# Optimization experiments

Hardware: AMD Instinct MI355X
Metric: run time of the kernel (lower is better)

Reference implementation:

```python
import jax, jax.numpy as jnp
import numpy as np
from jax import lax

B, C, H, W = 4096, 10, 30, 30
NCOL = C - 1                      # non-background colors 1..9
_pi, _pj = np.triu_indices(NCOL, 1)  # lexicographic (i<j) pair order, matches the python double loop
PI = jnp.asarray(_pi); PJ = jnp.asarray(_pj)
NPAIR = int(_pi.shape[0])         # 36
W_TRANSFORM, W_EXACT, W_AFFINE, W_ROT, W_REFL, W_GEO, W_EDGE, W_CBAL = 0.2, 7.0, 0.4, 0.3, 0.3, 0.5, 0.3, 0.2
GAMMA = 1.4


def setup_inputs() -> dict:
    key = jax.random.key(0)
    ks = jax.random.split(key, 6)
    pred = jax.random.normal(ks[0], (B, C, H, W), jnp.float32)
    tidx = jax.random.randint(ks[1], (B, H, W), 0, C)
    target = jnp.transpose(jax.nn.one_hot(tidx, C, dtype=jnp.float32), (0, 3, 1, 2))
    iidx = jax.random.randint(ks[2], (B, H, W), 0, C)
    input_grid = jnp.transpose(jax.nn.one_hot(iidx, C, dtype=jnp.float32), (0, 3, 1, 2))
    theta = 0.1 * jax.random.normal(ks[3], (B, 2, 3), jnp.float32)
    rot = jax.random.normal(ks[4], (B, 8), jnp.float32)
    refl = jax.random.normal(ks[5], (B, 4), jnp.float32)
    return {"pred_output": pred, "target_output": target, "input_grid": input_grid,
            "theta": theta, "rotation_logits": rot, "reflection_logits": refl}


def _detect_edges(idx):
    # idx: [B,H,W] int; pixel is an edge if it differs from any h/w neighbor
    dh = idx[:, 1:, :] != idx[:, :-1, :]
    dw = idx[:, :, 1:] != idx[:, :, :-1]
    e = jnp.pad(dh, ((0, 0), (1, 0), (0, 0))) | jnp.pad(dh, ((0, 0), (0, 1), (0, 0)))
    e = e | jnp.pad(dw, ((0, 0), (0, 0), (1, 0))) | jnp.pad(dw, ((0, 0), (0, 0), (0, 1)))
    return e


def _entropy_mean(logits):
    lp = jax.nn.log_softmax(logits, axis=1)
    return (-(jnp.exp(lp) * lp).sum(axis=1)).mean()


def _sobel(idx_f):
    sx = jnp.array([[-1., 0., 1.], [-2., 0., 2.], [-1., 0., 1.]], jnp.float32).reshape(1, 1, 3, 3)
    sy = jnp.array([[-1., -2., -1.], [0., 0., 0.], [1., 2., 1.]], jnp.float32).reshape(1, 1, 3, 3)
    x = idx_f[:, None]  # [B,1,H,W]
    dn = ('NCHW', 'OIHW', 'NCHW')
    ex = lax.conv_general_dilated(x, sx, (1, 1), ((1, 1), (1, 1)), dimension_numbers=dn)
    ey = lax.conv_general_dilated(x, sy, (1, 1), ((1, 1), (1, 1)), dimension_numbers=dn)
    return jnp.sqrt(ex * ex + ey * ey)


def _centers(grid):
    # grid: [H,W] int -> per-color (1..9) center of mass and presence
    cols = jnp.arange(1, C)
    mask = (grid[None] == cols[:, None, None]).astype(jnp.float32)  # [9,H,W]
    cnt = mask.sum((1, 2))
    ys = jnp.arange(H, dtype=jnp.float32)[:, None]
    xs = jnp.arange(W, dtype=jnp.float32)[None, :]
    cy = (mask * ys).sum((1, 2)) / jnp.maximum(cnt, 1.0)
    cx = (mask * xs).sum((1, 2)) / jnp.maximum(cnt, 1.0)
    return cy, cx, cnt > 0


def _compact_dists(cy, cx, present):
    # distances for all 36 color pairs, compacted so valid pairs occupy
    # the leading slots in the same lexicographic order as the torch loops
    d = jnp.sqrt((cy[PI] - cy[PJ]) ** 2 + (cx[PI] - cx[PJ]) ** 2)
    v = present[PI] & present[PJ]
    rank = jnp.cumsum(v.astype(jnp.int32)) - 1
    slot = jnp.where(v, rank, NPAIR)          # dump invalid pairs in scratch slot
    compact = jnp.zeros(NPAIR + 1, jnp.float32).at[slot].set(d)
    return compact[:NPAIR], v.sum()


def _geo_sample(pidx, tidx):
    cyp, cxp, prp = _centers(pidx)
    cyt, cxt, prt = _centers(tidx)
    dp, n_p = _compact_dists(cyp, cxp, prp)
    dt, n_t = _compact_dists(cyt, cxt, prt)
    m = jnp.minimum(n_p, n_t)                 # min_len truncation
    use = jnp.arange(NPAIR) < m
    sq = jnp.where(use, (dp - dt) ** 2, 0.0)
    return jnp.where(m > 0, sq.sum() / jnp.maximum(m, 1).astype(jnp.float32), 0.0)


def _components(pred, target, inp, theta, rot, refl):
    tidx = jnp.argmax(target, axis=1)
    pidx = jnp.argmax(pred, axis=1)
    iidx = jnp.argmax(inp, axis=1)
    # spatial focal CE with edge-weighted pixels
    lp = jax.nn.log_softmax(pred, axis=1)
    ce = -jnp.take_along_axis(lp, tidx[:, None], axis=1)[:, 0]  # [B,H,W]
    pt = jnp.exp(-ce)
    sw = jnp.where(_detect_edges(tidx), 1.5, 1.0)
    spatial_focal = ((1.0 - pt) ** GAMMA * ce * sw).mean()
    # exact match bonus / copy penalty
    exact = jnp.all(pidx == tidx, axis=(1, 2)).astype(jnp.float32)
    exact_count = exact.sum()
    exact_bonus = -exact.mean() * W_EXACT
    copy = jnp.all(pidx == iidx, axis=(1, 2)).astype(jnp.float32)
    transform = copy.mean() * W_TRANSFORM
    # affine regularization on theta
    scale_reg = jnp.sqrt((theta[:, :2, :2] ** 2).sum((1, 2)))
    trans_reg = jnp.sqrt((theta[:, :, 2] ** 2).sum(1))
    affine = (scale_reg.mean() + 0.1 * trans_reg.mean()) * W_AFFINE
    rotation = _entropy_mean(rot) * W_ROT
    reflection = _entropy_mean(refl) * W_REFL
    # geometric color-center consistency (vmapped over batch)
    geo = jax.vmap(_geo_sample)(pidx, tidx).sum() / B * W_GEO
    # sobel edge MSE on argmax indices
    pe = _sobel(pidx.astype(jnp.float32))
    te = _sobel(tidx.astype(jnp.float32))
    edge = jnp.mean((pe - te) ** 2) * W_EDGE
    # color balance
    pc = jax.nn.softmax(pred, axis=1).sum((2, 3))
    tc = target.sum((2, 3))
    pc = pc / (pc.sum(1, keepdims=True) + 1e-8)
    tc = tc / (tc.sum(1, keepdims=True) + 1e-8)
    cbal = jnp.mean((pc - tc) ** 2) * W_CBAL
    total = (spatial_focal + transform + affine + rotation + reflection
             + geo + edge + cbal + exact_bonus)
    return (total, spatial_focal, transform, exact_bonus, exact_count,
            affine, rotation, reflection, geo, edge, cbal)


def reference(pred_output, target_output, input_grid, theta, rotation_logits, reflection_logits):
    return _components(pred_output, target_output, input_grid, theta,
                       rotation_logits, reflection_logits)
```

## Files before the change

kernel.cpp:

```cpp
#include <hip/hip_runtime.h>
#include <stdint.h>

#define B_   4096
#define C_   10
#define H_   30
#define W_   30
#define HW_  900
#define NCOL_ 9
#define NPART 9

typedef float f32x4 __attribute__((ext_vector_type(4)));


__device__ __forceinline__ float entropyN(const float* __restrict__ x, int n) {
    float m = x[0];
    for (int i = 1; i < n; ++i) m = fmaxf(m, x[i]);
    float se = 0.f;
    for (int i = 0; i < n; ++i) se += __expf(x[i] - m);
    float lse = m + __logf(se);
    float ent = 0.f;
    for (int i = 0; i < n; ++i) { float lp = x[i] - lse; ent -= __expf(lp) * lp; }
    return ent;
}

template <int CTRL>
__device__ __forceinline__ float dpp_add_stage(float x) {
    int y = __builtin_amdgcn_update_dpp(0, __builtin_bit_cast(int, x),
                                        CTRL, 0xf, 0xf, true);
    return x + __builtin_bit_cast(float, y);
}
__device__ __forceinline__ float wave_sum64(float x) {
    x = dpp_add_stage<0x111>(x);
    x = dpp_add_stage<0x112>(x);
    x = dpp_add_stage<0x114>(x);
    x = dpp_add_stage<0x118>(x);
    x = dpp_add_stage<0x142>(x);
    x = dpp_add_stage<0x143>(x);
    return __builtin_bit_cast(float,
        __builtin_amdgcn_readlane(__builtin_bit_cast(int, x), 63));
}


__global__ __launch_bounds__(64) void zero_out_k(float* out, int n) {
    int i = threadIdx.x;
    if (i < n) out[i] = 0.f;
}

__global__ __launch_bounds__(256, 3) void loss_main(
    const float* __restrict__ pred, const float* __restrict__ target,
    const float* __restrict__ inp,  const float* __restrict__ theta,
    const float* __restrict__ rotl, const float* __restrict__ refl,
    float* __restrict__ partials ,
    float* __restrict__ out)
{
    __shared__ uint8_t s_t[33 * 32];
    __shared__ uint8_t s_p[33 * 32];
    __shared__ __align__(16) float s_fb[30 * 36];
    __shared__ unsigned long long s_ctr[2][NCOL_];
    __shared__ float s_wred[4][16];
    __shared__ float s_dp[36], s_dt[36];
    __shared__ float s_cy[2][NCOL_], s_cx[2][NCOL_];
    __shared__ int   s_pr[2][NCOL_];
    __shared__ int   s_tcnt[NCOL_];
    __shared__ float s_small[4];

    const int t    = threadIdx.x;
    const int wid  = t >> 6;
    const int lane = t & 63;
    const int b    = blockIdx.x;
    const size_t base = (size_t)b * (C_ * HW_);

    float pc[C_];
#pragma unroll
    for (int c = 0; c < C_; ++c) pc[c] = 0.f;
    float focal_base = 0.f, focal_edge = 0.f, edg = 0.f;
    bool ok_e = true, ok_c = true;

    if (t < 225) {
        const int p0 = 4 * t;
        const float* pp = pred   + base + p0;
        const float* tp = target + base + p0;
        const float* gp = inp    + base + p0;

        f32x4 pfv[C_], tfv[C_], gfv[C_];
#pragma unroll
        for (int c = 0; c < C_; ++c)
            asm volatile("global_load_dwordx4 %0, %1, off"
                         : "=v"(pfv[c]) : "v"(pp + c * HW_));
#pragma unroll
        for (int c = 0; c < C_; ++c)
            asm volatile("global_load_dwordx4 %0, %1, off"
                         : "=v"(tfv[c]) : "v"(tp + c * HW_));
#pragma unroll
        for (int c = 0; c < C_; ++c)
            asm volatile("global_load_dwordx4 %0, %1, off"
                         : "=v"(gfv[c]) : "v"(gp + c * HW_));
        asm volatile("s_waitcnt vmcnt(0)" ::: "memory");
        __builtin_amdgcn_sched_barrier(0);

        float vt[4]  = {0.f, 0.f, 0.f, 0.f};
        float tif[4] = {0.f, 0.f, 0.f, 0.f};
        float iif[4] = {0.f, 0.f, 0.f, 0.f};
#pragma unroll
        for (int c = 0; c < C_; ++c) {
            const f32x4 tf = tfv[c];
            const f32x4 pf = pfv[c];
            const f32x4 gf = gfv[c];
            const float fc = (float)c;
            vt[0] = fmaf(tf.x, pf.x, vt[0]); vt[1] = fmaf(tf.y, pf.y, vt[1]);
            vt[2] = fmaf(tf.z, pf.z, vt[2]); vt[3] = fmaf(tf.w, pf.w, vt[3]);
            tif[0] = fmaf(tf.x, fc, tif[0]); tif[1] = fmaf(tf.y, fc, tif[1]);
            tif[2] = fmaf(tf.z, fc, tif[2]); tif[3] = fmaf(tf.w, fc, tif[3]);
            iif[0] = fmaf(gf.x, fc, iif[0]); iif[1] = fmaf(gf.y, fc, iif[1]);
            iif[2] = fmaf(gf.z, fc, iif[2]); iif[3] = fmaf(gf.w, fc, iif[3]);
        }

        int h = p0 / 30;
        int w = p0 - 30 * h;
#pragma unroll
        for (int j = 0; j < 4; ++j) {
            const int ti = (int)tif[j];
            const int ii = (int)iif[j];
            float pm = pfv[0][j]; int pi = 0;
            float se = 0.f;
            float ex[C_];
#pragma unroll
            for (int c = 0; c < C_; ++c) {
                const float raw = pfv[c][j];
                if (c > 0 && raw > pm) { pm = raw; pi = c; }
                float e = __expf(raw);
                ex[c] = e;
                se += e;
            }
            const float inv = __builtin_amdgcn_rcpf(se);
#pragma unroll
            for (int c = 0; c < C_; ++c) pc[c] = fmaf(ex[c], inv, pc[c]);
            const float ce = __logf(se) - vt[j];
            const float pt = __expf(-ce);
            const float omt = fmaxf(1.f - pt, 0.f);
            const float fb = __powf(omt, 1.4f) * ce;
            focal_base += fb;

            s_t[(h + 1) * 32 + (w + 1)] = (uint8_t)ti;
            s_p[(h + 1) * 32 + (w + 1)] = (uint8_t)pi;
            s_fb[36 * h + w] = fb;
            if (pi != ti) ok_e = false;
            if (pi != ii) ok_c = false;
            if (++w == 30) { w = 0; ++h; }
        }
    } else if (t < 252) {
        const int z = t - 225;
        for (int k = z; k < 32; k += 27) {
            const int g = k >> 4, r = (k >> 3) & 1, dw = k & 7;
            uint32_t* pb = (uint32_t*)((g ? s_p : s_t) + (r ? 31 * 32 : 0));
            pb[dw] = 0u;
        }
        for (int k = z; k < 120; k += 27) {
            const int g = (k >= 60);
            const int kk = k - 60 * g;
            const int r = 1 + (kk >> 1);
            const int cp = (kk & 1) ? 31 : 0;
            (g ? s_p : s_t)[r * 32 + cp] = 0;
        }
        for (int k = z; k < 2 * NCOL_; k += 27) ((unsigned long long*)s_ctr)[k] = 0ull;
    } else if (t == 252) {
        s_small[0] = entropyN(rotl + (size_t)b * 8, 8);
    } else if (t == 253) {
        s_small[1] = entropyN(refl + (size_t)b * 4, 4);
    } else if (t == 254) {
        const float* th = theta + (size_t)b * 6;
        float sreg = sqrtf(th[0]*th[0] + th[1]*th[1] + th[3]*th[3] + th[4]*th[4]);
        float treg = sqrtf(th[2]*th[2] + th[5]*th[5]);
        s_small[2] = sreg + 0.1f * treg;
    }
    __syncthreads();

    if (t < 240) {
        const int h = t >> 3, wq = t & 7;
        const int w0 = 4 * wq;
        const int npx = (w0 < 28) ? 4 : 2;

        const uint32_t* tr0 = (const uint32_t*)(s_t + 32 * h);
        const uint32_t* tr1 = (const uint32_t*)(s_t + 32 * (h + 1));
        const uint32_t* tr2 = (const uint32_t*)(s_t + 32 * (h + 2));
        const uint32_t* pr0 = (const uint32_t*)(s_p + 32 * h);
        const uint32_t* pr1 = (const uint32_t*)(s_p + 32 * (h + 1));
        const uint32_t* pr2 = (const uint32_t*)(s_p + 32 * (h + 2));

        uint32_t td[3][2] = {{tr0[wq], tr0[wq + 1]}, {tr1[wq], tr1[wq + 1]}, {tr2[wq], tr2[wq + 1]}};
        uint32_t pd[3][2] = {{pr0[wq], pr0[wq + 1]}, {pr1[wq], pr1[wq + 1]}, {pr2[wq], pr2[wq + 1]}};
        const float4 fbf = *reinterpret_cast<const float4*>(s_fb + 36 * h + w0);
        const float fbarr[4] = {fbf.x, fbf.y, fbf.z, fbf.w};

        int tb2[3][6], pb2[3][6];
#pragma unroll
        for (int r = 0; r < 3; ++r) {
            const uint32_t d0t = td[r][0], d1t = td[r][1];
            tb2[r][0] = d0t & 255; tb2[r][1] = (d0t >> 8) & 255; tb2[r][2] = (d0t >> 16) & 255;
            tb2[r][3] = d0t >> 24; tb2[r][4] = d1t & 255; tb2[r][5] = (d1t >> 8) & 255;
            const uint32_t d0p = pd[r][0], d1p = pd[r][1];
            pb2[r][0] = d0p & 255; pb2[r][1] = (d0p >> 8) & 255; pb2[r][2] = (d0p >> 16) & 255;
            pb2[r][3] = d0p >> 24; pb2[r][4] = d1p & 255; pb2[r][5] = (d1p >> 8) & 255;
        }
        int s1t[6], s2t[6], s1p[6], s2p[6];
#pragma unroll
        for (int j = 0; j < 6; ++j) {
            s1t[j] = tb2[0][j] + 2 * tb2[1][j] + tb2[2][j];
            s2t[j] = tb2[2][j] - tb2[0][j];
            s1p[j] = pb2[0][j] + 2 * pb2[1][j] + pb2[2][j];
            s2p[j] = pb2[2][j] - pb2[0][j];
        }
#pragma unroll
        for (int k = 0; k < 4; ++k) {
            if (k < npx) {
                const int w = w0 + k;
                const int tv = tb2[1][k + 1], pv2 = pb2[1][k + 1];
                const bool eg = (h > 0  && tb2[0][k + 1] != tv) ||
                                (h < 29 && tb2[2][k + 1] != tv) ||
                                (w > 0  && tb2[1][k]     != tv) ||
                                (w < 29 && tb2[1][k + 2] != tv);
                if (eg) focal_edge += fbarr[k];

                const int ext = s1t[k + 2] - s1t[k];
                const int eyt = s2t[k] + 2 * s2t[k + 1] + s2t[k + 2];
                const int exq = s1p[k + 2] - s1p[k];
                const int eyq = s2p[k] + 2 * s2p[k + 1] + s2p[k + 2];
                const float mt = sqrtf((float)(ext * ext + eyt * eyt));
                const float mp = sqrtf((float)(exq * exq + eyq * eyq));
                const float dd = mp - mt;
                edg += dd * dd;

                const unsigned long long add =
                    (1ull << 42) | ((unsigned long long)(unsigned)h << 21) | (unsigned)w;
                if (tv  > 0) atomicAdd(&s_ctr[1][tv  - 1], add);
                if (pv2 > 0) atomicAdd(&s_ctr[0][pv2 - 1], add);
            }
        }
    }

    float vals[12];
    vals[0] = focal_base + 0.5f * focal_edge;
    vals[1] = edg;
#pragma unroll
    for (int c = 0; c < C_; ++c) vals[2 + c] = pc[c];
#pragma unroll
    for (int k = 0; k < 12; ++k) vals[k] = wave_sum64(vals[k]);
    const int all_e = __all(ok_e);
    const int all_c = __all(ok_c);
    if (lane == 0) {
#pragma unroll
        for (int k = 0; k < 12; ++k) s_wred[wid][k] = vals[k];
        s_wred[wid][12] = (float)all_e;
        s_wred[wid][13] = (float)all_c;
    }
    __syncthreads();

    if (t < 18) {
        const int g = (t >= 9);
        const int k = t - 9 * g;
        const unsigned long long q = s_ctr[g][k];
        const int sx = (int)(q & 0x1FFFFF), sy = (int)((q >> 21) & 0x1FFFFF), cn = (int)(q >> 42);
        const float dn = fmaxf((float)cn, 1.f);
        s_cy[g][k] = (float)sy / dn;
        s_cx[g][k] = (float)sx / dn;
        s_pr[g][k] = (cn > 0);
        if (g) s_tcnt[k] = cn;
    }
    __syncthreads();

    if (t < 64) {
        const int l = t;
        const int i = (l >= 8) + (l >= 15) + (l >= 21) + (l >= 26) +
                      (l >= 30) + (l >= 33) + (l >= 35);
        const int j = l - (i * (17 - i)) / 2 + i + 1;
        bool vp = false, vtp = false;
        float dp = 0.f, dt = 0.f;
        if (l < 36) {
            vp  = s_pr[0][i] && s_pr[0][j];
            vtp = s_pr[1][i] && s_pr[1][j];
            float dyp = s_cy[0][i] - s_cy[0][j], dxp = s_cx[0][i] - s_cx[0][j];
            dp = sqrtf(dyp * dyp + dxp * dxp);
            float dyt = s_cy[1][i] - s_cy[1][j], dxt = s_cx[1][i] - s_cx[1][j];
            dt = sqrtf(dyt * dyt + dxt * dxt);
        }
        const unsigned long long mp_mask = __ballot(vp);
        const unsigned long long mt_mask = __ballot(vtp);
        const unsigned long long below = (1ull << l) - 1ull;
        if (vp)  s_dp[__popcll(mp_mask & below)] = dp;
        if (vtp) s_dt[__popcll(mt_mask & below)] = dt;
        const int np = (int)__popcll(mp_mask);
        const int nt = (int)__popcll(mt_mask);
        const int mm = np < nt ? np : nt;
        asm volatile("s_waitcnt lgkmcnt(0)" ::: "memory");
        __builtin_amdgcn_wave_barrier();
        float term = 0.f;
        if (l < mm) { float d = s_dp[l] - s_dt[l]; term = d * d; }
#pragma unroll
        for (int off = 32; off > 0; off >>= 1) term += __shfl_down(term, off);

        if (t == 0) {
            const float geo_b = (mm > 0) ? term / (float)mm : 0.f;

            float r[14];
#pragma unroll
            for (int k = 0; k < 14; ++k) r[k] = s_wred[0][k];
            for (int w2 = 1; w2 < 4; ++w2) {
#pragma unroll
                for (int k = 0; k < 12; ++k) r[k] += s_wred[w2][k];
                r[12] = fminf(r[12], s_wred[w2][12]);
                r[13] = fminf(r[13], s_wred[w2][13]);
            }

            float pcs = 0.f;
#pragma unroll
            for (int c = 0; c < C_; ++c) pcs += r[2 + c];
            const float ipcs = 1.f / (pcs + 1e-8f);
            int tsum = 0;
#pragma unroll
            for (int k = 0; k < NCOL_; ++k) tsum += s_tcnt[k];
            float cb = 0.f;
            const float itd = 1.f / (900.f + 1e-8f);
            {
                float d = r[2] * ipcs - (float)(HW_ - tsum) * itd;
                cb += d * d;
            }
#pragma unroll
            for (int c = 1; c < C_; ++c) {
                float d = r[2 + c] * ipcs - (float)s_tcnt[c - 1] * itd;
                cb += d * d;
            }

            float res[NPART];
            res[0] = r[0];
            res[1] = r[12];
            res[2] = r[13];
            res[3] = s_small[2];
            res[4] = s_small[0];
            res[5] = s_small[1];
            res[6] = geo_b;
            res[7] = r[1];
            res[8] = cb;

            if (partials) {
                float* pw = partials + (size_t)b * NPART;
#pragma unroll
                for (int k = 0; k < NPART; ++k) pw[k] = res[k];
            } else {
                atomicAdd(&out[1],  res[0]);
                atomicAdd(&out[2],  res[2]);
                atomicAdd(&out[4],  res[1]);
                atomicAdd(&out[5],  res[3]);
                atomicAdd(&out[6],  res[4]);
                atomicAdd(&out[7],  res[5]);
                atomicAdd(&out[8],  res[6]);
                atomicAdd(&out[9],  res[7]);
                atomicAdd(&out[10], res[8]);
            }
        }
    }
}

__device__ __forceinline__ void write_final(float* out,
    double focal_s, double exact_s, double copy_s, double aff_s,
    double rot_s, double refl_s, double geo_s, double edge_s, double cbal_s)
{
    const double invB = 1.0 / (double)B_;
    float focal      = (float)(focal_s / ((double)B_ * (double)HW_));
    float transform  = (float)(copy_s * invB * 0.2);
    float exact_cnt  = (float)exact_s;
    float exact_bns  = (float)(-(exact_s * invB) * 7.0);
    float affine     = (float)(aff_s * invB * 0.4);
    float rotation   = (float)(rot_s * invB * 0.3);
    float reflection = (float)(refl_s * invB * 0.3);
    float geo        = (float)(geo_s * invB * 0.5);
    float edge       = (float)(edge_s / ((double)B_ * (double)HW_) * 0.3);
    float cbal       = (float)(cbal_s / ((double)B_ * (double)C_) * 0.2);
    out[0] = focal + transform + affine + rotation + reflection + geo + edge + cbal + exact_bns;
    out[1] = focal; out[2] = transform; out[3] = exact_bns; out[4] = exact_cnt;
    out[5] = affine; out[6] = rotation; out[7] = reflection; out[8] = geo;
    out[9] = edge; out[10] = cbal;
}

__global__ __launch_bounds__(256) void reduce_partials(
    const float* __restrict__ partials, float* __restrict__ out)
{
    __shared__ double sh[256][NPART];
    const int t = threadIdx.x;
    double acc[NPART];
#pragma unroll
    for (int k = 0; k < NPART; ++k) acc[k] = 0.0;
    for (int b = t; b < B_; b += 256) {
        const float* pp = partials + (size_t)b * NPART;
#pragma unroll
        for (int k = 0; k < NPART; ++k) acc[k] += (double)pp[k];
    }
#pragma unroll
    for (int k = 0; k < NPART; ++k) sh[t][k] = acc[k];
    __syncthreads();
    for (int s = 128; s > 0; s >>= 1) {
        if (t < s) {
#pragma unroll
            for (int k = 0; k < NPART; ++k) sh[t][k] += sh[t + s][k];
        }
        __syncthreads();
    }
    if (t == 0) {
        write_final(out, sh[0][0], sh[0][1], sh[0][2], sh[0][3],
                    sh[0][4], sh[0][5], sh[0][6], sh[0][7], sh[0][8]);
    }
}

__global__ void finalize_atomic(float* out) {
    if (threadIdx.x == 0) {
        write_final(out, (double)out[1], (double)out[4], (double)out[2], (double)out[5],
                    (double)out[6], (double)out[7], (double)out[8], (double)out[9],
                    (double)out[10]);
    }
}


extern "C" void kernel_launch(void* const* d_in, const int* in_sizes, int n_in,
                              void* d_out, int out_size, void* d_ws, size_t ws_size,
                              hipStream_t stream) {
    const float* pred   = (const float*)d_in[0];
    const float* target = (const float*)d_in[1];
    const float* inp    = (const float*)d_in[2];
    const float* theta  = (const float*)d_in[3];
    const float* rotl   = (const float*)d_in[4];
    const float* refl   = (const float*)d_in[5];
    float* out = (float*)d_out;

    const size_t need = (size_t)B_ * NPART * sizeof(float);
    if (d_ws != nullptr && ws_size >= need) {
        loss_main<<<B_, 256, 0, stream>>>(pred, target, inp, theta, rotl, refl,
                                          (float*)d_ws, out);
        reduce_partials<<<1, 256, 0, stream>>>((const float*)d_ws, out);
    } else {
        zero_out_k<<<1, 64, 0, stream>>>(out, out_size);
        loss_main<<<B_, 256, 0, stream>>>(pred, target, inp, theta, rotl, refl,
                                          nullptr, out);
        finalize_atomic<<<1, 1, 0, stream>>>(out);
    }
}
```

Baseline: 89.65 us.

## Process four batch elements per block with prefetch of next element's loads

Each block now handles four batch samples in a loop. As soon as the per-pixel phase of one sample finishes, it issues the global loads for the next sample, so those loads overlap the stencil, atomic and reduction phases. Loads are split so pred and target are waited on first and the input grid later. The launch bound drops to two blocks per CU and the grid shrinks by four. This trades fewer resident blocks and more register pressure for overlap on what is likely a bandwidth-bound kernel.

```diff
diff --git a/kernel.cpp b/kernel.cpp
--- a/kernel.cpp
+++ b/kernel.cpp
@@ -1,13 +1,14 @@
 #include <hip/hip_runtime.h>
 #include <stdint.h>
 
-#define B_   4096
-#define C_   10
-#define H_   30
-#define W_   30
-#define HW_  900
+#define B_    4096
+#define C_    10
+#define H_    30
+#define W_    30
+#define HW_   900
 #define NCOL_ 9
 #define NPART 9
+#define ELEMS 4
 
 typedef float f32x4 __attribute__((ext_vector_type(4)));
 
@@ -46,7 +47,7 @@
     if (i < n) out[i] = 0.f;
 }
 
-__global__ __launch_bounds__(256, 3) void loss_main(
+__global__ __launch_bounds__(256, 2) void loss_main(
     const float* __restrict__ pred, const float* __restrict__ target,
     const float* __restrict__ inp,  const float* __restrict__ theta,
     const float* __restrict__ rotl, const float* __restrict__ refl,
@@ -62,27 +63,20 @@
     __shared__ float s_cy[2][NCOL_], s_cx[2][NCOL_];
     __shared__ int   s_pr[2][NCOL_];
     __shared__ int   s_tcnt[NCOL_];
-    __shared__ float s_small[4];
+    __shared__ float s_small[ELEMS][4];
 
     const int t    = threadIdx.x;
     const int wid  = t >> 6;
     const int lane = t & 63;
-    const int b    = blockIdx.x;
-    const size_t base = (size_t)b * (C_ * HW_);
-
-    float pc[C_];
-#pragma unroll
-    for (int c = 0; c < C_; ++c) pc[c] = 0.f;
-    float focal_base = 0.f, focal_edge = 0.f, edg = 0.f;
-    bool ok_e = true, ok_c = true;
-
-    if (t < 225) {
-        const int p0 = 4 * t;
-        const float* pp = pred   + base + p0;
-        const float* tp = target + base + p0;
-        const float* gp = inp    + base + p0;
-
-        f32x4 pfv[C_], tfv[C_], gfv[C_];
+    const int b0   = blockIdx.x * ELEMS;
+    const int p0   = 4 * t;
+
+    f32x4 pfv[C_], tfv[C_], gfv[C_];
+
+    auto issue = [&](size_t bs) {
+        const float* pp = pred   + bs + p0;
+        const float* tp = target + bs + p0;
+        const float* gp = inp    + bs + p0;
 #pragma unroll
         for (int c = 0; c < C_; ++c)
             asm volatile("global_load_dwordx4 %0, %1, off"
@@ -95,59 +89,10 @@
         for (int c = 0; c < C_; ++c)
             asm volatile("global_load_dwordx4 %0, %1, off"
                          : "=v"(gfv[c]) : "v"(gp + c * HW_));
-        asm volatile("s_waitcnt vmcnt(0)" ::: "memory");
-        __builtin_amdgcn_sched_barrier(0);
-
-        float vt[4]  = {0.f, 0.f, 0.f, 0.f};
-        float tif[4] = {0.f, 0.f, 0.f, 0.f};
-        float iif[4] = {0.f, 0.f, 0.f, 0.f};
-#pragma unroll
-        for (int c = 0; c < C_; ++c) {
-            const f32x4 tf = tfv[c];
-            const f32x4 pf = pfv[c];
-            const f32x4 gf = gfv[c];
-            const float fc = (float)c;
-            vt[0] = fmaf(tf.x, pf.x, vt[0]); vt[1] = fmaf(tf.y, pf.y, vt[1]);
-            vt[2] = fmaf(tf.z, pf.z, vt[2]); vt[3] = fmaf(tf.w, pf.w, vt[3]);
-            tif[0] = fmaf(tf.x, fc, tif[0]); tif[1] = fmaf(tf.y, fc, tif[1]);
-            tif[2] = fmaf(tf.z, fc, tif[2]); tif[3] = fmaf(tf.w, fc, tif[3]);
-            iif[0] = fmaf(gf.x, fc, iif[0]); iif[1] = fmaf(gf.y, fc, iif[1]);
-            iif[2] = fmaf(gf.z, fc, iif[2]); iif[3] = fmaf(gf.w, fc, iif[3]);
-        }
-
-        int h = p0 / 30;
-        int w = p0 - 30 * h;
-#pragma unroll
-        for (int j = 0; j < 4; ++j) {
-            const int ti = (int)tif[j];
-            const int ii = (int)iif[j];
-            float pm = pfv[0][j]; int pi = 0;
-            float se = 0.f;
-            float ex[C_];
-#pragma unroll
-            for (int c = 0; c < C_; ++c) {
-                const float raw = pfv[c][j];
-                if (c > 0 && raw > pm) { pm = raw; pi = c; }
-                float e = __expf(raw);
-                ex[c] = e;
-                se += e;
-            }
-            const float inv = __builtin_amdgcn_rcpf(se);
-#pragma unroll
-            for (int c = 0; c < C_; ++c) pc[c] = fmaf(ex[c], inv, pc[c]);
-            const float ce = __logf(se) - vt[j];
-            const float pt = __expf(-ce);
-            const float omt = fmaxf(1.f - pt, 0.f);
-            const float fb = __powf(omt, 1.4f) * ce;
-            focal_base += fb;
-
-            s_t[(h + 1) * 32 + (w + 1)] = (uint8_t)ti;
-            s_p[(h + 1) * 32 + (w + 1)] = (uint8_t)pi;
-            s_fb[36 * h + w] = fb;
-            if (pi != ti) ok_e = false;
-            if (pi != ii) ok_c = false;
-            if (++w == 30) { w = 0; ++h; }
-        }
+    };
+
+    if (t < 225) {
+        issue((size_t)b0 * (C_ * HW_));
     } else if (t < 252) {
         const int z = t - 225;
         for (int k = z; k < 32; k += 27) {
@@ -162,199 +107,287 @@
             const int cp = (kk & 1) ? 31 : 0;
             (g ? s_p : s_t)[r * 32 + cp] = 0;
         }
-        for (int k = z; k < 2 * NCOL_; k += 27) ((unsigned long long*)s_ctr)[k] = 0ull;
     } else if (t == 252) {
-        s_small[0] = entropyN(rotl + (size_t)b * 8, 8);
+#pragma unroll
+        for (int e = 0; e < ELEMS; ++e)
+            s_small[e][0] = entropyN(rotl + (size_t)(b0 + e) * 8, 8);
     } else if (t == 253) {
-        s_small[1] = entropyN(refl + (size_t)b * 4, 4);
+#pragma unroll
+        for (int e = 0; e < ELEMS; ++e)
+            s_small[e][1] = entropyN(refl + (size_t)(b0 + e) * 4, 4);
     } else if (t == 254) {
-        const float* th = theta + (size_t)b * 6;
-        float sreg = sqrtf(th[0]*th[0] + th[1]*th[1] + th[3]*th[3] + th[4]*th[4]);
-        float treg = sqrtf(th[2]*th[2] + th[5]*th[5]);
-        s_small[2] = sreg + 0.1f * treg;
-    }
-    __syncthreads();
-
-    if (t < 240) {
-        const int h = t >> 3, wq = t & 7;
-        const int w0 = 4 * wq;
-        const int npx = (w0 < 28) ? 4 : 2;
-
-        const uint32_t* tr0 = (const uint32_t*)(s_t + 32 * h);
-        const uint32_t* tr1 = (const uint32_t*)(s_t + 32 * (h + 1));
-        const uint32_t* tr2 = (const uint32_t*)(s_t + 32 * (h + 2));
-        const uint32_t* pr0 = (const uint32_t*)(s_p + 32 * h);
-        const uint32_t* pr1 = (const uint32_t*)(s_p + 32 * (h + 1));
-        const uint32_t* pr2 = (const uint32_t*)(s_p + 32 * (h + 2));
-
-        uint32_t td[3][2] = {{tr0[wq], tr0[wq + 1]}, {tr1[wq], tr1[wq + 1]}, {tr2[wq], tr2[wq + 1]}};
-        uint32_t pd[3][2] = {{pr0[wq], pr0[wq + 1]}, {pr1[wq], pr1[wq + 1]}, {pr2[wq], pr2[wq + 1]}};
-        const float4 fbf = *reinterpret_cast<const float4*>(s_fb + 36 * h + w0);
-        const float fbarr[4] = {fbf.x, fbf.y, fbf.z, fbf.w};
-
-        int tb2[3][6], pb2[3][6];
-#pragma unroll
-        for (int r = 0; r < 3; ++r) {
-            const uint32_t d0t = td[r][0], d1t = td[r][1];
-            tb2[r][0] = d0t & 255; tb2[r][1] = (d0t >> 8) & 255; tb2[r][2] = (d0t >> 16) & 255;
-            tb2[r][3] = d0t >> 24; tb2[r][4] = d1t & 255; tb2[r][5] = (d1t >> 8) & 255;
-            const uint32_t d0p = pd[r][0], d1p = pd[r][1];
-            pb2[r][0] = d0p & 255; pb2[r][1] = (d0p >> 8) & 255; pb2[r][2] = (d0p >> 16) & 255;
-            pb2[r][3] = d0p >> 24; pb2[r][4] = d1p & 255; pb2[r][5] = (d1p >> 8) & 255;
-        }
-        int s1t[6], s2t[6], s1p[6], s2p[6];
-#pragma unroll
-        for (int j = 0; j < 6; ++j) {
-            s1t[j] = tb2[0][j] + 2 * tb2[1][j] + tb2[2][j];
-            s2t[j] = tb2[2][j] - tb2[0][j];
-            s1p[j] = pb2[0][j] + 2 * pb2[1][j] + pb2[2][j];
-            s2p[j] = pb2[2][j] - pb2[0][j];
-        }
-#pragma unroll
-        for (int k = 0; k < 4; ++k) {
-            if (k < npx) {
-                const int w = w0 + k;
-                const int tv = tb2[1][k + 1], pv2 = pb2[1][k + 1];
-                const bool eg = (h > 0  && tb2[0][k + 1] != tv) ||
-                                (h < 29 && tb2[2][k + 1] != tv) ||
-                                (w > 0  && tb2[1][k]     != tv) ||
-                                (w < 29 && tb2[1][k + 2] != tv);
-                if (eg) focal_edge += fbarr[k];
-
-                const int ext = s1t[k + 2] - s1t[k];
-                const int eyt = s2t[k] + 2 * s2t[k + 1] + s2t[k + 2];
-                const int exq = s1p[k + 2] - s1p[k];
-                const int eyq = s2p[k] + 2 * s2p[k + 1] + s2p[k + 2];
-                const float mt = sqrtf((float)(ext * ext + eyt * eyt));
-                const float mp = sqrtf((float)(exq * exq + eyq * eyq));
-                const float dd = mp - mt;
-                edg += dd * dd;
-
-                const unsigned long long add =
-                    (1ull << 42) | ((unsigned long long)(unsigned)h << 21) | (unsigned)w;
-                if (tv  > 0) atomicAdd(&s_ctr[1][tv  - 1], add);
-                if (pv2 > 0) atomicAdd(&s_ctr[0][pv2 - 1], add);
-            }
-        }
-    }
-
-    float vals[12];
-    vals[0] = focal_base + 0.5f * focal_edge;
-    vals[1] = edg;
-#pragma unroll
-    for (int c = 0; c < C_; ++c) vals[2 + c] = pc[c];
-#pragma unroll
-    for (int k = 0; k < 12; ++k) vals[k] = wave_sum64(vals[k]);
-    const int all_e = __all(ok_e);
-    const int all_c = __all(ok_c);
-    if (lane == 0) {
-#pragma unroll
-        for (int k = 0; k < 12; ++k) s_wred[wid][k] = vals[k];
-        s_wred[wid][12] = (float)all_e;
-        s_wred[wid][13] = (float)all_c;
-    }
-    __syncthreads();
-
-    if (t < 18) {
-        const int g = (t >= 9);
-        const int k = t - 9 * g;
-        const unsigned long long q = s_ctr[g][k];
-        const int sx = (int)(q & 0x1FFFFF), sy = (int)((q >> 21) & 0x1FFFFF), cn = (int)(q >> 42);
-        const float dn = fmaxf((float)cn, 1.f);
-        s_cy[g][k] = (float)sy / dn;
-        s_cx[g][k] = (float)sx / dn;
-        s_pr[g][k] = (cn > 0);
-        if (g) s_tcnt[k] = cn;
-    }
-    __syncthreads();
-
-    if (t < 64) {
-        const int l = t;
-        const int i = (l >= 8) + (l >= 15) + (l >= 21) + (l >= 26) +
-                      (l >= 30) + (l >= 33) + (l >= 35);
-        const int j = l - (i * (17 - i)) / 2 + i + 1;
-        bool vp = false, vtp = false;
-        float dp = 0.f, dt = 0.f;
-        if (l < 36) {
-            vp  = s_pr[0][i] && s_pr[0][j];
-            vtp = s_pr[1][i] && s_pr[1][j];
-            float dyp = s_cy[0][i] - s_cy[0][j], dxp = s_cx[0][i] - s_cx[0][j];
-            dp = sqrtf(dyp * dyp + dxp * dxp);
-            float dyt = s_cy[1][i] - s_cy[1][j], dxt = s_cx[1][i] - s_cx[1][j];
-            dt = sqrtf(dyt * dyt + dxt * dxt);
-        }
-        const unsigned long long mp_mask = __ballot(vp);
-        const unsigned long long mt_mask = __ballot(vtp);
-        const unsigned long long below = (1ull << l) - 1ull;
-        if (vp)  s_dp[__popcll(mp_mask & below)] = dp;
-        if (vtp) s_dt[__popcll(mt_mask & below)] = dt;
-        const int np = (int)__popcll(mp_mask);
-        const int nt = (int)__popcll(mt_mask);
-        const int mm = np < nt ? np : nt;
-        asm volatile("s_waitcnt lgkmcnt(0)" ::: "memory");
-        __builtin_amdgcn_wave_barrier();
-        float term = 0.f;
-        if (l < mm) { float d = s_dp[l] - s_dt[l]; term = d * d; }
-#pragma unroll
-        for (int off = 32; off > 0; off >>= 1) term += __shfl_down(term, off);
-
-        if (t == 0) {
-            const float geo_b = (mm > 0) ? term / (float)mm : 0.f;
-
-            float r[14];
-#pragma unroll
-            for (int k = 0; k < 14; ++k) r[k] = s_wred[0][k];
-            for (int w2 = 1; w2 < 4; ++w2) {
-#pragma unroll
-                for (int k = 0; k < 12; ++k) r[k] += s_wred[w2][k];
-                r[12] = fminf(r[12], s_wred[w2][12]);
-                r[13] = fminf(r[13], s_wred[w2][13]);
-            }
-
-            float pcs = 0.f;
-#pragma unroll
-            for (int c = 0; c < C_; ++c) pcs += r[2 + c];
-            const float ipcs = 1.f / (pcs + 1e-8f);
-            int tsum = 0;
-#pragma unroll
-            for (int k = 0; k < NCOL_; ++k) tsum += s_tcnt[k];
-            float cb = 0.f;
-            const float itd = 1.f / (900.f + 1e-8f);
-            {
-                float d = r[2] * ipcs - (float)(HW_ - tsum) * itd;
-                cb += d * d;
-            }
-#pragma unroll
-            for (int c = 1; c < C_; ++c) {
-                float d = r[2 + c] * ipcs - (float)s_tcnt[c - 1] * itd;
-                cb += d * d;
-            }
-
-            float res[NPART];
-            res[0] = r[0];
-            res[1] = r[12];
-            res[2] = r[13];
-            res[3] = s_small[2];
-            res[4] = s_small[0];
-            res[5] = s_small[1];
-            res[6] = geo_b;
-            res[7] = r[1];
-            res[8] = cb;
-
-            if (partials) {
-                float* pw = partials + (size_t)b * NPART;
-#pragma unroll
-                for (int k = 0; k < NPART; ++k) pw[k] = res[k];
-            } else {
-                atomicAdd(&out[1],  res[0]);
-                atomicAdd(&out[2],  res[2]);
-                atomicAdd(&out[4],  res[1]);
-                atomicAdd(&out[5],  res[3]);
-                atomicAdd(&out[6],  res[4]);
-                atomicAdd(&out[7],  res[5]);
-                atomicAdd(&out[8],  res[6]);
-                atomicAdd(&out[9],  res[7]);
-                atomicAdd(&out[10], res[8]);
+#pragma unroll
+        for (int e = 0; e < ELEMS; ++e) {
+            const float* th = theta + (size_t)(b0 + e) * 6;
+            float sreg = sqrtf(th[0]*th[0] + th[1]*th[1] + th[3]*th[3] + th[4]*th[4]);
+            float treg = sqrtf(th[2]*th[2] + th[5]*th[5]);
+            s_small[e][2] = sreg + 0.1f * treg;
+        }
+    }
+
+#pragma unroll 1
+    for (int e = 0; e < ELEMS; ++e) {
+        float pc[C_];
+#pragma unroll
+        for (int c = 0; c < C_; ++c) pc[c] = 0.f;
+        float focal_base = 0.f, focal_edge = 0.f, edg = 0.f;
+        bool ok_e = true, ok_c = true;
+
+        if (t < 225) {
+            asm volatile("s_waitcnt vmcnt(10)" ::: "memory");
+            __builtin_amdgcn_sched_barrier(0);
+
+            float vt[4]  = {0.f, 0.f, 0.f, 0.f};
+            float tif[4] = {0.f, 0.f, 0.f, 0.f};
+#pragma unroll
+            for (int c = 0; c < C_; ++c) {
+                const f32x4 tf = tfv[c];
+                const f32x4 pf = pfv[c];
+                const float fc = (float)c;
+                vt[0] = fmaf(tf.x, pf.x, vt[0]); vt[1] = fmaf(tf.y, pf.y, vt[1]);
+                vt[2] = fmaf(tf.z, pf.z, vt[2]); vt[3] = fmaf(tf.w, pf.w, vt[3]);
+                tif[0] = fmaf(tf.x, fc, tif[0]); tif[1] = fmaf(tf.y, fc, tif[1]);
+                tif[2] = fmaf(tf.z, fc, tif[2]); tif[3] = fmaf(tf.w, fc, tif[3]);
+            }
+
+            int ti4[4], pi4[4];
+            int h = p0 / 30;
+            int w = p0 - 30 * h;
+#pragma unroll
+            for (int j = 0; j < 4; ++j) {
+                const int ti = (int)tif[j];
+                ti4[j] = ti;
+                float pm = pfv[0][j]; int pi = 0;
+                float se = 0.f;
+                float ex[C_];
+#pragma unroll
+                for (int c = 0; c < C_; ++c) {
+                    const float raw = pfv[c][j];
+                    if (c > 0 && raw > pm) { pm = raw; pi = c; }
+                    float eo = __expf(raw);
+                    ex[c] = eo;
+                    se += eo;
+                }
+                pi4[j] = pi;
+                const float inv = __builtin_amdgcn_rcpf(se);
+#pragma unroll
+                for (int c = 0; c < C_; ++c) pc[c] = fmaf(ex[c], inv, pc[c]);
+                const float ce = __logf(se) - vt[j];
+                const float pt = __expf(-ce);
+                const float omt = fmaxf(1.f - pt, 0.f);
+                const float fb = __powf(omt, 1.4f) * ce;
+                focal_base += fb;
+
+                s_t[(h + 1) * 32 + (w + 1)] = (uint8_t)ti;
+                s_p[(h + 1) * 32 + (w + 1)] = (uint8_t)pi;
+                s_fb[36 * h + w] = fb;
+                if (pi != ti) ok_e = false;
+                if (++w == 30) { w = 0; ++h; }
+            }
+
+            asm volatile("s_waitcnt vmcnt(0)" ::: "memory");
+            __builtin_amdgcn_sched_barrier(0);
+            float iif[4] = {0.f, 0.f, 0.f, 0.f};
+#pragma unroll
+            for (int c = 0; c < C_; ++c) {
+                const f32x4 gf = gfv[c];
+                const float fc = (float)c;
+                iif[0] = fmaf(gf.x, fc, iif[0]); iif[1] = fmaf(gf.y, fc, iif[1]);
+                iif[2] = fmaf(gf.z, fc, iif[2]); iif[3] = fmaf(gf.w, fc, iif[3]);
+            }
+#pragma unroll
+            for (int j = 0; j < 4; ++j)
+                if (pi4[j] != (int)iif[j]) ok_c = false;
+
+            if (e + 1 < ELEMS)
+                issue((size_t)(b0 + e + 1) * (C_ * HW_));
+        } else {
+            const int z = t - 225;
+            if (z < 2 * NCOL_) ((unsigned long long*)s_ctr)[z] = 0ull;
+        }
+        __syncthreads();
+
+        if (t < 240) {
+            const int h = t >> 3, wq = t & 7;
+            const int w0 = 4 * wq;
+            const int npx = (w0 < 28) ? 4 : 2;
+
+            const uint32_t* tr0 = (const uint32_t*)(s_t + 32 * h);
+            const uint32_t* tr1 = (const uint32_t*)(s_t + 32 * (h + 1));
+            const uint32_t* tr2 = (const uint32_t*)(s_t + 32 * (h + 2));
+            const uint32_t* pr0 = (const uint32_t*)(s_p + 32 * h);
+            const uint32_t* pr1 = (const uint32_t*)(s_p + 32 * (h + 1));
+            const uint32_t* pr2 = (const uint32_t*)(s_p + 32 * (h + 2));
+
+            uint32_t td[3][2] = {{tr0[wq], tr0[wq + 1]}, {tr1[wq], tr1[wq + 1]}, {tr2[wq], tr2[wq + 1]}};
+            uint32_t pd[3][2] = {{pr0[wq], pr0[wq + 1]}, {pr1[wq], pr1[wq + 1]}, {pr2[wq], pr2[wq + 1]}};
+            const float4 fbf = *reinterpret_cast<const float4*>(s_fb + 36 * h + w0);
+            const float fbarr[4] = {fbf.x, fbf.y, fbf.z, fbf.w};
+
+            int tb2[3][6], pb2[3][6];
+#pragma unroll
+            for (int r = 0; r < 3; ++r) {
+                const uint32_t d0t = td[r][0], d1t = td[r][1];
+                tb2[r][0] = d0t & 255; tb2[r][1] = (d0t >> 8) & 255; tb2[r][2] = (d0t >> 16) & 255;
+                tb2[r][3] = d0t >> 24; tb2[r][4] = d1t & 255; tb2[r][5] = (d1t >> 8) & 255;
+                const uint32_t d0p = pd[r][0], d1p = pd[r][1];
+                pb2[r][0] = d0p & 255; pb2[r][1] = (d0p >> 8) & 255; pb2[r][2] = (d0p >> 16) & 255;
+                pb2[r][3] = d0p >> 24; pb2[r][4] = d1p & 255; pb2[r][5] = (d1p >> 8) & 255;
+            }
+            int s1t[6], s2t[6], s1p[6], s2p[6];
+#pragma unroll
+            for (int j = 0; j < 6; ++j) {
+                s1t[j] = tb2[0][j] + 2 * tb2[1][j] + tb2[2][j];
+                s2t[j] = tb2[2][j] - tb2[0][j];
+                s1p[j] = pb2[0][j] + 2 * pb2[1][j] + pb2[2][j];
+                s2p[j] = pb2[2][j] - pb2[0][j];
+            }
+#pragma unroll
+            for (int k = 0; k < 4; ++k) {
+                if (k < npx) {
+                    const int w = w0 + k;
+                    const int tv = tb2[1][k + 1], pv2 = pb2[1][k + 1];
+                    const bool eg = (h > 0  && tb2[0][k + 1] != tv) ||
+                                    (h < 29 && tb2[2][k + 1] != tv) ||
+                                    (w > 0  && tb2[1][k]     != tv) ||
+                                    (w < 29 && tb2[1][k + 2] != tv);
+                    if (eg) focal_edge += fbarr[k];
+
+                    const int ext = s1t[k + 2] - s1t[k];
+                    const int eyt = s2t[k] + 2 * s2t[k + 1] + s2t[k + 2];
+                    const int exq = s1p[k + 2] - s1p[k];
+                    const int eyq = s2p[k] + 2 * s2p[k + 1] + s2p[k + 2];
+                    const float mt = sqrtf((float)(ext * ext + eyt * eyt));
+                    const float mp = sqrtf((float)(exq * exq + eyq * eyq));
+                    const float dd = mp - mt;
+                    edg += dd * dd;
+
+                    const unsigned long long add =
+                        (1ull << 42) | ((unsigned long long)(unsigned)h << 21) | (unsigned)w;
+                    if (tv  > 0) atomicAdd(&s_ctr[1][tv  - 1], add);
+                    if (pv2 > 0) atomicAdd(&s_ctr[0][pv2 - 1], add);
+                }
+            }
+        }
+
+        float vals[12];
+        vals[0] = focal_base + 0.5f * focal_edge;
+        vals[1] = edg;
+#pragma unroll
+        for (int c = 0; c < C_; ++c) vals[2 + c] = pc[c];
+#pragma unroll
+        for (int k = 0; k < 12; ++k) vals[k] = wave_sum64(vals[k]);
+        const int all_e = __all(ok_e);
+        const int all_c = __all(ok_c);
+        if (lane == 0) {
+#pragma unroll
+            for (int k = 0; k < 12; ++k) s_wred[wid][k] = vals[k];
+            s_wred[wid][12] = (float)all_e;
+            s_wred[wid][13] = (float)all_c;
+        }
+        __syncthreads();
+
+        if (t < 18) {
+            const int g = (t >= 9);
+            const int k = t - 9 * g;
+            const unsigned long long q = s_ctr[g][k];
+            const int sx = (int)(q & 0x1FFFFF), sy = (int)((q >> 21) & 0x1FFFFF), cn = (int)(q >> 42);
+            const float dn = fmaxf((float)cn, 1.f);
+            s_cy[g][k] = (float)sy / dn;
+            s_cx[g][k] = (float)sx / dn;
+            s_pr[g][k] = (cn > 0);
+            if (g) s_tcnt[k] = cn;
+        }
+        __syncthreads();
+
+        if (t < 64) {
+            const int l = t;
+            const int i = (l >= 8) + (l >= 15) + (l >= 21) + (l >= 26) +
+                          (l >= 30) + (l >= 33) + (l >= 35);
+            const int j = l - (i * (17 - i)) / 2 + i + 1;
+            bool vp = false, vtp = false;
+            float dp = 0.f, dt = 0.f;
+            if (l < 36) {
+                vp  = s_pr[0][i] && s_pr[0][j];
+                vtp = s_pr[1][i] && s_pr[1][j];
+                float dyp = s_cy[0][i] - s_cy[0][j], dxp = s_cx[0][i] - s_cx[0][j];
+                dp = sqrtf(dyp * dyp + dxp * dxp);
+                float dyt = s_cy[1][i] - s_cy[1][j], dxt = s_cx[1][i] - s_cx[1][j];
+                dt = sqrtf(dyt * dyt + dxt * dxt);
+            }
+            const unsigned long long mp_mask = __ballot(vp);
+            const unsigned long long mt_mask = __ballot(vtp);
+            const unsigned long long below = (1ull << l) - 1ull;
+            if (vp)  s_dp[__popcll(mp_mask & below)] = dp;
+            if (vtp) s_dt[__popcll(mt_mask & below)] = dt;
+            const int np = (int)__popcll(mp_mask);
+            const int nt = (int)__popcll(mt_mask);
+            const int mm = np < nt ? np : nt;
+            asm volatile("s_waitcnt lgkmcnt(0)" ::: "memory");
+            __builtin_amdgcn_wave_barrier();
+            float term = 0.f;
+            if (l < mm) { float d = s_dp[l] - s_dt[l]; term = d * d; }
+#pragma unroll
+            for (int off = 32; off > 0; off >>= 1) term += __shfl_down(term, off);
+
+            if (t == 0) {
+                const float geo_b = (mm > 0) ? term / (float)mm : 0.f;
+
+                float r[14];
+#pragma unroll
+                for (int k = 0; k < 14; ++k) r[k] = s_wred[0][k];
+                for (int w2 = 1; w2 < 4; ++w2) {
+#pragma unroll
+                    for (int k = 0; k < 12; ++k) r[k] += s_wred[w2][k];
+                    r[12] = fminf(r[12], s_wred[w2][12]);
+                    r[13] = fminf(r[13], s_wred[w2][13]);
+                }
+
+                float pcs = 0.f;
+#pragma unroll
+                for (int c = 0; c < C_; ++c) pcs += r[2 + c];
+                const float ipcs = 1.f / (pcs + 1e-8f);
+                int tsum = 0;
+#pragma unroll
+                for (int k = 0; k < NCOL_; ++k) tsum += s_tcnt[k];
+                float cb = 0.f;
+                const float itd = 1.f / (900.f + 1e-8f);
+                {
+                    float d = r[2] * ipcs - (float)(HW_ - tsum) * itd;
+                    cb += d * d;
+                }
+#pragma unroll
+                for (int c = 1; c < C_; ++c) {
+                    float d = r[2 + c] * ipcs - (float)s_tcnt[c - 1] * itd;
+                    cb += d * d;
+                }
+
+                float res[NPART];
+                res[0] = r[0];
+                res[1] = r[12];
+                res[2] = r[13];
+                res[3] = s_small[e][2];
+                res[4] = s_small[e][0];
+                res[5] = s_small[e][1];
+                res[6] = geo_b;
+                res[7] = r[1];
+                res[8] = cb;
+
+                if (partials) {
+                    float* pw = partials + (size_t)(b0 + e) * NPART;
+#pragma unroll
+                    for (int k = 0; k < NPART; ++k) pw[k] = res[k];
+                } else {
+                    atomicAdd(&out[1],  res[0]);
+                    atomicAdd(&out[2],  res[2]);
+                    atomicAdd(&out[4],  res[1]);
+                    atomicAdd(&out[5],  res[3]);
+                    atomicAdd(&out[6],  res[4]);
+                    atomicAdd(&out[7],  res[5]);
+                    atomicAdd(&out[8],  res[6]);
+                    atomicAdd(&out[9],  res[7]);
+                    atomicAdd(&out[10], res[8]);
+                }
             }
         }
     }
@@ -432,13 +465,13 @@
 
     const size_t need = (size_t)B_ * NPART * sizeof(float);
     if (d_ws != nullptr && ws_size >= need) {
-        loss_main<<<B_, 256, 0, stream>>>(pred, target, inp, theta, rotl, refl,
-                                          (float*)d_ws, out);
+        loss_main<<<B_ / ELEMS, 256, 0, stream>>>(pred, target, inp, theta, rotl, refl,
+                                                  (float*)d_ws, out);
         reduce_partials<<<1, 256, 0, stream>>>((const float*)d_ws, out);
     } else {
         zero_out_k<<<1, 64, 0, stream>>>(out, out_size);
-        loss_main<<<B_, 256, 0, stream>>>(pred, target, inp, theta, rotl, refl,
-                                          nullptr, out);
+        loss_main<<<B_ / ELEMS, 256, 0, stream>>>(pred, target, inp, theta, rotl, refl,
+                                                  nullptr, out);
         finalize_atomic<<<1, 1, 0, stream>>>(out);
     }
 }
```

Measured after the change: 101.9 us. 1.14x slower.
